# Performance work log

Hardware: AMD Instinct MI355X
Metric: run time of the kernel (lower is better)

Reference implementation:

```python
import jax, jax.numpy as jnp
import numpy as np

B = 262144          # flattened batch of (sample, time) points
D = 16              # input_dim: number of independent per-dimension MLPs
TE = 3              # time_embedding_dim -> per-dim MLP input width = 1 + TE = 4
H = 64              # hidden width (model_dims = [64, 64, 1])


def setup_inputs() -> dict:
    key = jax.random.key(0)
    ks = jax.random.split(key, 8)
    s1 = 1.0 / np.sqrt(1 + TE)   # torch nn.Linear default init scale ~ U(-1/sqrt(fan_in), ...)
    s2 = 1.0 / np.sqrt(H)
    return {
        "t": jax.random.normal(ks[0], (B, TE), jnp.float32),
        "y": jax.random.normal(ks[1], (B, D), jnp.float32),
        # stacked per-dim weights: layer l weight [D, in_l, out_l], bias [D, out_l]
        "W1": jax.random.uniform(ks[2], (D, 1 + TE, H), jnp.float32, -s1, s1),
        "b1": jax.random.uniform(ks[3], (D, H), jnp.float32, -s1, s1),
        "W2": jax.random.uniform(ks[4], (D, H, H), jnp.float32, -s2, s2),
        "b2": jax.random.uniform(ks[5], (D, H), jnp.float32, -s2, s2),
        "W3": jax.random.uniform(ks[6], (D, H, 1), jnp.float32, -s2, s2),
        "b3": jax.random.uniform(ks[7], (D, 1), jnp.float32, -s2, s2),
    }


def reference(t, y, W1, b1, W2, b2, W3, b3):
    # Per-dim MLP input: concat([y_i, t]) -> [B, D, 1+TE]
    Bn, Dn = y.shape
    x = jnp.concatenate(
        [y[:, :, None], jnp.broadcast_to(t[:, None, :], (Bn, Dn, t.shape[-1]))], axis=-1
    )
    h = jax.nn.softplus(jnp.einsum("bdi,dih->bdh", x, W1) + b1)      # Linear + Softplus
    h = jax.nn.softplus(jnp.einsum("bdh,dhk->bdk", h, W2) + b2)      # Linear + Softplus
    out = jnp.einsum("bdk,dko->bdo", h, W3) + b3                      # final Linear, out=1
    # concat over D then final activation: [B, D]
    return jax.nn.softplus(out[..., 0])
```

## Files before the change

### kernel.cpp

```cpp
#include <hip/hip_runtime.h>
#include <cmath>

#define B_TOTAL 262144
#define D 16
#define TE 3
#define H 64

#define TPB 16
#define NBX (B_TOTAL / 16 / TPB)
#define NBY 4

#define LOG2E 1.44269504088896340736f
#define LN2   0.693147180559945309417f

#define RSH 72
#define ARS 10

typedef _Float16 half8  __attribute__((ext_vector_type(8)));
typedef _Float16 half4  __attribute__((ext_vector_type(4)));
typedef __fp16   fp16x2 __attribute__((ext_vector_type(2)));
typedef float    f32x4  __attribute__((ext_vector_type(4)));
typedef unsigned int uint32;

__device__ __forceinline__ float sp_log2(float xs) {
    return __builtin_amdgcn_logf(1.0f + __builtin_amdgcn_exp2f(xs));
}
__device__ __forceinline__ float softplus_full(float x) {
    float e = __builtin_amdgcn_exp2f(-fabsf(x) * LOG2E);
    return fmaxf(x, 0.0f) + LN2 * __builtin_amdgcn_logf(1.0f + e);
}

__global__ __launch_bounds__(256, 4) void DiagonalVariance_kernel(
    const float* __restrict__ t,
    const float* __restrict__ y,
    const float* __restrict__ W1,
    const float* __restrict__ b1,
    const float* __restrict__ W2,
    const float* __restrict__ b2,
    const float* __restrict__ W3,
    const float* __restrict__ b3,
    float* __restrict__ out)
{
    __shared__ __align__(16) _Float16 tbuf[4 * 16 * RSH];
    __shared__ __align__(16) float obuf[TPB * 16 * 4];
    __shared__ __align__(16) uint32 abuf[256 * ARS];

    const int wave = threadIdx.x >> 6;
    const int lane = threadIdx.x & 63;
    const int q    = lane >> 4;
    const int lm   = lane & 15;
    const int d    = blockIdx.y * 4 + wave;
    const bool q0  = (q == 0);

    {
        const int i    = threadIdx.x;
        const int grow = blockIdx.x * 256 + i;
        const f32x4 yv = *(const f32x4*)(y + grow * D + blockIdx.y * 4);
        const float* tpp = t + grow * TE;
        const float tt0 = tpp[0], tt1 = tpp[1], tt2 = tpp[2];
        const uint32 u1 = __builtin_bit_cast(uint32, __builtin_amdgcn_cvt_pkrtz(tt1, tt2));
        uint32* ab = abuf + i * ARS;
        ab[0] = __builtin_bit_cast(uint32, __builtin_amdgcn_cvt_pkrtz(yv.x, tt0)); ab[1] = u1;
        ab[2] = __builtin_bit_cast(uint32, __builtin_amdgcn_cvt_pkrtz(yv.y, tt0)); ab[3] = u1;
        ab[4] = __builtin_bit_cast(uint32, __builtin_amdgcn_cvt_pkrtz(yv.z, tt0)); ab[5] = u1;
        ab[6] = __builtin_bit_cast(uint32, __builtin_amdgcn_cvt_pkrtz(yv.w, tt0)); ab[7] = u1;
    }

    const float* __restrict__ W1d = W1 + d * (4 * H);
    const float* __restrict__ b1d = b1 + d * H;
    const float* __restrict__ W2d = W2 + d * (H * H);
    const float* __restrict__ b2d = b2 + d * H;
    const float* __restrict__ W3d = W3 + d * H;

    half8 w2f[2][4];
    #pragma unroll
    for (int ks = 0; ks < 2; ++ks)
        #pragma unroll
        for (int nt = 0; nt < 4; ++nt)
            #pragma unroll
            for (int j = 0; j < 8; ++j)
                w2f[ks][nt][j] = (_Float16)W2d[(32 * ks + 8 * q + j) * H + 16 * nt + lm];

    half4 w1f[4];
    #pragma unroll
    for (int nt = 0; nt < 4; ++nt) {
        #pragma unroll
        for (int i = 0; i < 4; ++i) {
            const int h = 16 * nt + lm;
            float v = 0.0f;
            if (q == 0)           v = W1d[i * H + h] * LOG2E;
            if (q == 1 && i == 0) v = b1d[h] * LOG2E;
            w1f[nt][i] = (_Float16)v;
        }
    }

    half8 w3f[2];
    #pragma unroll
    for (int ks = 0; ks < 2; ++ks)
        #pragma unroll
        for (int j = 0; j < 8; ++j)
            w3f[ks][j] = (_Float16)(W3d[32 * ks + 8 * q + j] * LN2);

    const f32x4 ZC = {0.f, 0.f, 0.f, 0.f};
    f32x4 b2c[4];
    #pragma unroll
    for (int nt = 0; nt < 4; ++nt) {
        const float v = b2d[16 * nt + lm] * LOG2E;
        b2c[nt] = (f32x4){v, v, v, v};
    }
    const float b3s = b3[d];
    const f32x4 b3c = {b3s, b3s, b3s, b3s};

    _Float16* const tb  = tbuf + wave * (16 * RSH);
    _Float16* const twr = tb + (q * 4) * RSH + lm;
    const _Float16* const trd = tb + lm * RSH + 8 * q;

    const uint32* const ard = abuf + lm * ARS + 2 * wave;

    __syncthreads();

    #pragma unroll 1
    for (int tg = 0; tg < TPB; ++tg) {
        const uint32 a0 = ard[tg * 16 * ARS + 0];
        const uint32 a1 = ard[tg * 16 * ARS + 1];
        union { half4 h; uint32 u[2]; } af;
        af.u[0] = q0 ? a0 : 0x00003C00u;
        af.u[1] = q0 ? a1 : 0u;

        f32x4 acc1[4];
        #pragma unroll
        for (int nt = 0; nt < 4; ++nt)
            acc1[nt] = __builtin_amdgcn_mfma_f32_16x16x16f16(af.h, w1f[nt], ZC, 0, 0, 0);

        #pragma unroll
        for (int nt = 0; nt < 4; ++nt) {
            const fp16x2 p01 = __builtin_amdgcn_cvt_pkrtz(sp_log2(acc1[nt][0]),
                                                          sp_log2(acc1[nt][1]));
            const fp16x2 p23 = __builtin_amdgcn_cvt_pkrtz(sp_log2(acc1[nt][2]),
                                                          sp_log2(acc1[nt][3]));
            __fp16* const wb = (__fp16*)(twr + nt * 16);
            wb[0 * RSH] = p01.x;
            wb[1 * RSH] = p01.y;
            wb[2 * RSH] = p23.x;
            wb[3 * RSH] = p23.y;
        }

        half8 a2[2];
        #pragma unroll
        for (int ks = 0; ks < 2; ++ks)
            a2[ks] = *(const half8*)(trd + 32 * ks);

        f32x4 acc2[4];
        #pragma unroll
        for (int nt = 0; nt < 4; ++nt)
            acc2[nt] = __builtin_amdgcn_mfma_f32_16x16x32_f16(a2[0], w2f[0][nt], b2c[nt], 0, 0, 0);
        #pragma unroll
        for (int nt = 0; nt < 4; ++nt)
            acc2[nt] = __builtin_amdgcn_mfma_f32_16x16x32_f16(a2[1], w2f[1][nt], acc2[nt], 0, 0, 0);

        #pragma unroll
        for (int nt = 0; nt < 4; ++nt) {
            const fp16x2 p01 = __builtin_amdgcn_cvt_pkrtz(sp_log2(acc2[nt][0]),
                                                          sp_log2(acc2[nt][1]));
            const fp16x2 p23 = __builtin_amdgcn_cvt_pkrtz(sp_log2(acc2[nt][2]),
                                                          sp_log2(acc2[nt][3]));
            __fp16* const wb = (__fp16*)(twr + nt * 16);
            wb[0 * RSH] = p01.x;
            wb[1 * RSH] = p01.y;
            wb[2 * RSH] = p23.x;
            wb[3 * RSH] = p23.y;
        }

        half8 a3[2];
        #pragma unroll
        for (int ks = 0; ks < 2; ++ks)
            a3[ks] = *(const half8*)(trd + 32 * ks);

        f32x4 acc3;
        acc3 = __builtin_amdgcn_mfma_f32_16x16x32_f16(a3[0], w3f[0], b3c, 0, 0, 0);
        acc3 = __builtin_amdgcn_mfma_f32_16x16x32_f16(a3[1], w3f[1], acc3, 0, 0, 0);

        const float v01 = (lm & 1) ? acc3[1] : acc3[0];
        const float v23 = (lm & 1) ? acc3[3] : acc3[2];
        const float vs  = (lm & 2) ? v23 : v01;
        if (lm < 4)
            obuf[(tg * 16 + q * 4 + lm) * 4 + wave] = vs;
    }

    __syncthreads();
    const int i = threadIdx.x;
    f32x4 v = *(const f32x4*)(obuf + 4 * i);
    v.x = softplus_full(v.x);
    v.y = softplus_full(v.y);
    v.z = softplus_full(v.z);
    v.w = softplus_full(v.w);
    *(f32x4*)(out + (blockIdx.x * 256 + i) * D + blockIdx.y * 4) = v;
}

extern "C" void kernel_launch(void* const* d_in, const int* in_sizes, int n_in,
                              void* d_out, int out_size, void* d_ws, size_t ws_size,
                              hipStream_t stream) {
    const float* t  = (const float*)d_in[0];
    const float* y  = (const float*)d_in[1];
    const float* W1 = (const float*)d_in[2];
    const float* b1 = (const float*)d_in[3];
    const float* W2 = (const float*)d_in[4];
    const float* b2 = (const float*)d_in[5];
    const float* W3 = (const float*)d_in[6];
    const float* b3 = (const float*)d_in[7];
    float* out = (float*)d_out;

    DiagonalVariance_kernel<<<dim3(NBX, NBY), dim3(256), 0, stream>>>(
        t, y, W1, b1, W2, b2, W3, b3, out);
}
```

Baseline: 197.5 us.

## Fuse final linear layer into layer-2 epilogue via FMA and lane swizzle reduction

Swaps the layer-2 MFMA operands so each lane holds hidden units for a sample column. This lets the width-1 output layer be computed with per-lane FMAs against preloaded W3 values, followed by a ds_swizzle pair reduction and a two-slot LDS partial sum. It removes the second LDS write/read round trip and the output-layer MFMAs, and it software-prefetches the next tile's input from LDS. In exchange, obuf doubles in size and there is extra reduction work in the tail.

```diff
diff --git a/kernel.cpp b/kernel.cpp
--- a/kernel.cpp
+++ b/kernel.cpp
@@ -15,6 +15,8 @@
 
 #define RSH 72
 #define ARS 10
+
+#define OSTRIDE (TPB * 16 * 4)
 
 typedef _Float16 half8  __attribute__((ext_vector_type(8)));
 typedef _Float16 half4  __attribute__((ext_vector_type(4)));
@@ -42,7 +44,7 @@
     float* __restrict__ out)
 {
     __shared__ __align__(16) _Float16 tbuf[4 * 16 * RSH];
-    __shared__ __align__(16) float obuf[TPB * 16 * 4];
+    __shared__ __align__(16) float obuf[2 * OSTRIDE];
     __shared__ __align__(16) uint32 abuf[256 * ARS];
 
     const int wave = threadIdx.x >> 6;
@@ -94,22 +96,22 @@
         }
     }
 
-    half8 w3f[2];
-    #pragma unroll
-    for (int ks = 0; ks < 2; ++ks)
-        #pragma unroll
-        for (int j = 0; j < 8; ++j)
-            w3f[ks][j] = (_Float16)(W3d[32 * ks + 8 * q + j] * LN2);
-
     const f32x4 ZC = {0.f, 0.f, 0.f, 0.f};
     f32x4 b2c[4];
     #pragma unroll
     for (int nt = 0; nt < 4; ++nt) {
-        const float v = b2d[16 * nt + lm] * LOG2E;
-        b2c[nt] = (f32x4){v, v, v, v};
-    }
-    const float b3s = b3[d];
-    const f32x4 b3c = {b3s, b3s, b3s, b3s};
+        f32x4 bv = *(const f32x4*)(b2d + 16 * nt + 4 * q);
+        b2c[nt] = (f32x4){bv.x * LOG2E, bv.y * LOG2E, bv.z * LOG2E, bv.w * LOG2E};
+    }
+
+    f32x4 w3l[4];
+    #pragma unroll
+    for (int nt = 0; nt < 4; ++nt) {
+        f32x4 wv = *(const f32x4*)(W3d + 16 * nt + 4 * q);
+        w3l[nt] = (f32x4){wv.x * LN2, wv.y * LN2, wv.z * LN2, wv.w * LN2};
+    }
+
+    const float sInit = ((lane & 48) == 0) ? b3[d] : 0.0f;
 
     _Float16* const tb  = tbuf + wave * (16 * RSH);
     _Float16* const twr = tb + (q * 4) * RSH + lm;
@@ -119,10 +121,18 @@
 
     __syncthreads();
 
+    uint32 a0n = ard[0];
+    uint32 a1n = ard[1];
+
     #pragma unroll 1
     for (int tg = 0; tg < TPB; ++tg) {
-        const uint32 a0 = ard[tg * 16 * ARS + 0];
-        const uint32 a1 = ard[tg * 16 * ARS + 1];
+        const uint32 a0 = a0n;
+        const uint32 a1 = a1n;
+        {
+            const int tn = (tg + 1 < TPB) ? (tg + 1) : tg;
+            a0n = ard[tn * 16 * ARS + 0];
+            a1n = ard[tn * 16 * ARS + 1];
+        }
         union { half4 h; uint32 u[2]; } af;
         af.u[0] = q0 ? a0 : 0x00003C00u;
         af.u[1] = q0 ? a1 : 0u;
@@ -153,47 +163,36 @@
         f32x4 acc2[4];
         #pragma unroll
         for (int nt = 0; nt < 4; ++nt)
-            acc2[nt] = __builtin_amdgcn_mfma_f32_16x16x32_f16(a2[0], w2f[0][nt], b2c[nt], 0, 0, 0);
-        #pragma unroll
-        for (int nt = 0; nt < 4; ++nt)
-            acc2[nt] = __builtin_amdgcn_mfma_f32_16x16x32_f16(a2[1], w2f[1][nt], acc2[nt], 0, 0, 0);
-
+            acc2[nt] = __builtin_amdgcn_mfma_f32_16x16x32_f16(w2f[0][nt], a2[0], b2c[nt], 0, 0, 0);
+        #pragma unroll
+        for (int nt = 0; nt < 4; ++nt)
+            acc2[nt] = __builtin_amdgcn_mfma_f32_16x16x32_f16(w2f[1][nt], a2[1], acc2[nt], 0, 0, 0);
+
+        float s0 = sInit, s1 = 0.0f;
         #pragma unroll
         for (int nt = 0; nt < 4; ++nt) {
-            const fp16x2 p01 = __builtin_amdgcn_cvt_pkrtz(sp_log2(acc2[nt][0]),
-                                                          sp_log2(acc2[nt][1]));
-            const fp16x2 p23 = __builtin_amdgcn_cvt_pkrtz(sp_log2(acc2[nt][2]),
-                                                          sp_log2(acc2[nt][3]));
-            __fp16* const wb = (__fp16*)(twr + nt * 16);
-            wb[0 * RSH] = p01.x;
-            wb[1 * RSH] = p01.y;
-            wb[2 * RSH] = p23.x;
-            wb[3 * RSH] = p23.y;
-        }
-
-        half8 a3[2];
-        #pragma unroll
-        for (int ks = 0; ks < 2; ++ks)
-            a3[ks] = *(const half8*)(trd + 32 * ks);
-
-        f32x4 acc3;
-        acc3 = __builtin_amdgcn_mfma_f32_16x16x32_f16(a3[0], w3f[0], b3c, 0, 0, 0);
-        acc3 = __builtin_amdgcn_mfma_f32_16x16x32_f16(a3[1], w3f[1], acc3, 0, 0, 0);
-
-        const float v01 = (lm & 1) ? acc3[1] : acc3[0];
-        const float v23 = (lm & 1) ? acc3[3] : acc3[2];
-        const float vs  = (lm & 2) ? v23 : v01;
-        if (lm < 4)
-            obuf[(tg * 16 + q * 4 + lm) * 4 + wave] = vs;
+            s0 = fmaf(sp_log2(acc2[nt][0]), w3l[nt][0], s0);
+            s1 = fmaf(sp_log2(acc2[nt][1]), w3l[nt][1], s1);
+            s0 = fmaf(sp_log2(acc2[nt][2]), w3l[nt][2], s0);
+            s1 = fmaf(sp_log2(acc2[nt][3]), w3l[nt][3], s1);
+        }
+        float s = s0 + s1;
+        const uint32 sw = (uint32)__builtin_amdgcn_ds_swizzle(
+            (int)__builtin_bit_cast(uint32, s), 0x401F);
+        s += __builtin_bit_cast(float, sw);
+        if ((lane & 16) == 0)
+            obuf[(lane >> 5) * OSTRIDE + (tg * 16 + lm) * 4 + wave] = s;
     }
 
     __syncthreads();
     const int i = threadIdx.x;
-    f32x4 v = *(const f32x4*)(obuf + 4 * i);
-    v.x = softplus_full(v.x);
-    v.y = softplus_full(v.y);
-    v.z = softplus_full(v.z);
-    v.w = softplus_full(v.w);
+    const f32x4 va = *(const f32x4*)(obuf + 4 * i);
+    const f32x4 vb = *(const f32x4*)(obuf + OSTRIDE + 4 * i);
+    f32x4 v;
+    v.x = softplus_full(va.x + vb.x);
+    v.y = softplus_full(va.y + vb.y);
+    v.z = softplus_full(va.z + vb.z);
+    v.w = softplus_full(va.w + vb.w);
     *(f32x4*)(out + (blockIdx.x * 256 + i) * D + blockIdx.y * 4) = v;
 }
 
```

New measurement: 192.6 us. 1.03x faster.
